# Performance work log

Measured on AMD Instinct MI355X. Metric: run time of the kernel, lower is better.

Reference implementation:

```python
import jax, jax.numpy as jnp
import numpy as np

B, S, E, H, A, D, V, L = 64, 196, 512, 512, 256, 512, 32000, 32
PAD_IDX = 2


def setup_inputs() -> dict:
    key = jax.random.key(0)
    ks = jax.random.split(key, 20)
    sc = 0.02
    return {
        "encoder_out": jax.random.normal(ks[0], (B, S, E), jnp.float32),
        "pooled": jax.random.normal(ks[1], (B, E), jnp.float32),
        "targets": jax.random.randint(ks[2], (B, L), 0, V, jnp.int64),
        "embedding": jax.random.normal(ks[3], (V, D), jnp.float32) * sc,
        "W_enc": jax.random.normal(ks[4], (A, E), jnp.float32) * sc,
        "b_enc": jnp.zeros((A,), jnp.float32),
        "W_dec": jax.random.normal(ks[5], (A, H), jnp.float32) * sc,
        "b_dec": jnp.zeros((A,), jnp.float32),
        "W_score": jax.random.normal(ks[6], (1, A), jnp.float32) * sc,
        "b_score": jnp.zeros((1,), jnp.float32),
        "W_ih": jax.random.normal(ks[7], (3 * H, D + E), jnp.float32) * sc,
        "W_hh": jax.random.normal(ks[8], (3 * H, H), jnp.float32) * sc,
        "b_ih": jnp.zeros((3 * H,), jnp.float32),
        "b_hh": jnp.zeros((3 * H,), jnp.float32),
        "W_out": jax.random.normal(ks[9], (V, H), jnp.float32) * sc,
        "b_out": jnp.zeros((V,), jnp.float32),
        "W_init": jax.random.normal(ks[10], (H, E), jnp.float32) * sc,
        "b_init": jnp.zeros((H,), jnp.float32),
    }


def reference(encoder_out, pooled, targets, embedding, W_enc, b_enc, W_dec,
              b_dec, W_score, b_score, W_ih, W_hh, b_ih, b_hh, W_out, b_out,
              W_init, b_init):
    # padding_idx=2: that embedding row is zero
    emb_tab = embedding.at[PAD_IDX].set(0.0)
    # initial hidden state from pooled features
    h0 = jnp.tanh(pooled @ W_init.T + b_init)              # (B, H)
    # encoder projection is step-invariant; hoist out of the loop
    enc_proj = jnp.einsum('bse,ae->bsa', encoder_out, W_enc) + b_enc  # (B,S,A)
    # teacher forcing (ratio=1.0): inputs are targets[:, :-1]
    tokens = targets[:, :-1].T                              # (L-1, B)

    def step(h, tok):
        embedded = emb_tab[tok]                             # (B, D)
        # Bahdanau attention
        dec_proj = h @ W_dec.T + b_dec                      # (B, A)
        energy = jnp.tanh(enc_proj + dec_proj[:, None, :])  # (B, S, A)
        scores = jnp.einsum('bsa,a->bs', energy, W_score[0]) + b_score[0]
        weights = jax.nn.softmax(scores, axis=1)            # (B, S)
        context = jnp.einsum('bs,bse->be', weights, encoder_out)  # (B, E)
        # GRU cell (PyTorch gate ordering: r, z, n)
        x = jnp.concatenate([embedded, context], axis=1)    # (B, D+E)
        gi = x @ W_ih.T + b_ih                              # (B, 3H)
        gh = h @ W_hh.T + b_hh                              # (B, 3H)
        gi_r, gi_z, gi_n = jnp.split(gi, 3, axis=1)
        gh_r, gh_z, gh_n = jnp.split(gh, 3, axis=1)
        r = jax.nn.sigmoid(gi_r + gh_r)
        z = jax.nn.sigmoid(gi_z + gh_z)
        n = jnp.tanh(gi_n + r * gh_n)
        h_new = (1.0 - z) * n + z * h
        logits = h_new @ W_out.T + b_out                    # (B, V)
        return h_new, logits

    _, logits = jax.lax.scan(step, h0, tokens)              # (L-1, B, V)
    return jnp.transpose(logits, (1, 0, 2))                 # (B, L-1, V)
```

## Files before the change

kernel.cpp:

```cpp
#include <hip/hip_runtime.h>

using bf16x8 = __attribute__((ext_vector_type(8))) short;
using f32x4  = __attribute__((ext_vector_type(4))) float;

__device__ inline float bf2f(unsigned short h){
  union { unsigned int u; float f; } v; v.u = ((unsigned int)h) << 16; return v.f;
}
__device__ inline unsigned short f2b(float x){
  union { float f; unsigned int u; } v; v.f = x;
  unsigned int r = (v.u + 0x7FFFu + ((v.u >> 16) & 1u)) >> 16;
  return (unsigned short)r;
}

__global__ void conv_k(const float* __restrict__ s, unsigned short* __restrict__ d, int n){
  int i = (blockIdx.x * 256 + threadIdx.x) * 4;
  if (i >= n) return;
  float4 v = *(const float4*)(s + i);
  unsigned int p0 = (unsigned int)f2b(v.x) | ((unsigned int)f2b(v.y) << 16);
  unsigned int p1 = (unsigned int)f2b(v.z) | ((unsigned int)f2b(v.w) << 16);
  *(uint2*)(d + i) = make_uint2(p0, p1);
}

__global__ void embed_k(const int* __restrict__ tgt, const float* __restrict__ emb,
                        unsigned short* __restrict__ out, int n){
  int idx = blockIdx.x * 256 + threadIdx.x;
  if (idx >= n) return;
  int d = idx & 511, m = idx >> 9, t = m >> 6, b = m & 63;
  int tok = tgt[b * 32 + t];
  float v = (tok == 2) ? 0.f : emb[(long)tok * 512 + d];
  out[idx] = f2b(v);
}

#define EPI_PLAIN 0
#define EPI_TANH  1
#define EPI_OUT   2

template<int EPI, bool AF32>
__global__ __launch_bounds__(256)
void gemm_bt(const void* __restrict__ Av, int lda,
             const unsigned short* __restrict__ Bp, int ldb,
             const float* __restrict__ bias,
             float* __restrict__ Cf, unsigned short* __restrict__ Cb, int ldc,
             int K,
             int n_split, const void* __restrict__ A2v,
             const unsigned short* __restrict__ B2p, int lda2, int ldb2)
{
  __shared__ __align__(16) unsigned short As[64][40];
  __shared__ __align__(16) unsigned short Bs[256][40];

  int m0 = blockIdx.x * 64;
  int n0 = blockIdx.y * 256;
  const void* Ap = Av; const unsigned short* Bq = Bp;
  int la = lda, lb = ldb, nB = n0;
  if (n_split > 0 && n0 >= n_split){ Ap = A2v; Bq = B2p; la = lda2; lb = ldb2; nB = n0 - n_split; }

  int tid  = threadIdx.x;
  int wave = tid >> 6, lane = tid & 63, quad = lane >> 4, lrow = lane & 15;

  f32x4 acc[4][4];
#pragma unroll
  for (int i = 0; i < 4; ++i)
#pragma unroll
    for (int j = 0; j < 4; ++j)
#pragma unroll
      for (int r = 0; r < 4; ++r) acc[i][j][r] = 0.f;

  int ar = tid >> 2, ac = (tid & 3) * 8;

  for (int k0 = 0; k0 < K; k0 += 32){
    if (AF32){
      const float* A32 = (const float*)Ap;
      const float4* src = (const float4*)(A32 + (long)(m0 + ar) * la + k0 + ac);
      float4 x0 = src[0], x1 = src[1];
      unsigned int p0 = (unsigned int)f2b(x0.x) | ((unsigned int)f2b(x0.y) << 16);
      unsigned int p1 = (unsigned int)f2b(x0.z) | ((unsigned int)f2b(x0.w) << 16);
      unsigned int p2 = (unsigned int)f2b(x1.x) | ((unsigned int)f2b(x1.y) << 16);
      unsigned int p3 = (unsigned int)f2b(x1.z) | ((unsigned int)f2b(x1.w) << 16);
      *(uint4*)&As[ar][ac] = make_uint4(p0, p1, p2, p3);
    } else {
      const unsigned short* A16 = (const unsigned short*)Ap;
      *(uint4*)&As[ar][ac] = *(const uint4*)(A16 + (long)(m0 + ar) * la + k0 + ac);
    }
#pragma unroll
    for (int c = 0; c < 4; ++c){
      int id = tid + c * 256; int br = id >> 2, bc = (id & 3) * 8;
      *(uint4*)&Bs[br][bc] = *(const uint4*)(Bq + (long)(nB + br) * lb + k0 + bc);
    }
    __syncthreads();

    bf16x8 af[4], bfr[4];
#pragma unroll
    for (int mf = 0; mf < 4; ++mf) af[mf]  = *(const bf16x8*)&As[mf * 16 + lrow][quad * 8];
#pragma unroll
    for (int nf = 0; nf < 4; ++nf) bfr[nf] = *(const bf16x8*)&Bs[wave * 64 + nf * 16 + lrow][quad * 8];
#pragma unroll
    for (int mf = 0; mf < 4; ++mf)
#pragma unroll
      for (int nf = 0; nf < 4; ++nf)
        acc[mf][nf] = __builtin_amdgcn_mfma_f32_16x16x32_bf16(af[mf], bfr[nf], acc[mf][nf], 0, 0, 0);
    __syncthreads();
  }

#pragma unroll
  for (int mf = 0; mf < 4; ++mf){
#pragma unroll
    for (int nf = 0; nf < 4; ++nf){
#pragma unroll
      for (int r = 0; r < 4; ++r){
        int m = m0 + mf * 16 + quad * 4 + r;
        int n = n0 + wave * 64 + nf * 16 + lrow;
        float v = acc[mf][nf][r];
        if (bias) v += bias[n];
        if (EPI == EPI_TANH){
          v = tanhf(v);
          Cf[(long)m * ldc + n] = v;
          Cb[(long)m * ldc + n] = f2b(v);
        } else if (EPI == EPI_OUT){
          Cf[(long)(m & 63) * (31 * 32000) + (long)(m >> 6) * 32000 + n] = v;
        } else {
          Cf[(long)m * ldc + n] = v;
        }
      }
    }
  }
}

__global__ __launch_bounds__(512)
void attn_step(const float* __restrict__ enc_proj,
               const float* __restrict__ enc_out,
               const float* __restrict__ W_score,
               const float* __restrict__ b_dec,
               const float* __restrict__ b_hh,
               const float* __restrict__ gi_emb,
               const float* __restrict__ giq,
               float* __restrict__ h_all,
               unsigned short* __restrict__ h_b16,
               const unsigned short* __restrict__ Wdec,
               unsigned short* __restrict__ ctx_b16,
               int t, int do_gates, int do_attn)
{
  int b = blockIdx.x, tid = threadIdx.x;
  __shared__ float sh_h[512];
  __shared__ float sdp[256];
  __shared__ float sbuf[512];
  __shared__ float sw[256];
  __shared__ float sred[512];
  __shared__ float swsc[256];

  float hv;
  if (do_gates){
    int j = tid;
    long ge = ((long)(t - 1) * 64 + b) * 1536;
    long gq = (long)b * 3072;
    float gir = gi_emb[ge + j]        + giq[gq + j];
    float giz = gi_emb[ge + 512 + j]  + giq[gq + 512 + j];
    float gin = gi_emb[ge + 1024 + j] + giq[gq + 1024 + j];
    float ghr = giq[gq + 1536 + j]        + b_hh[j];
    float ghz = giq[gq + 1536 + 512 + j]  + b_hh[512 + j];
    float ghn = giq[gq + 1536 + 1024 + j] + b_hh[1024 + j];
    float rr = 1.f / (1.f + __expf(-(gir + ghr)));
    float zz = 1.f / (1.f + __expf(-(giz + ghz)));
    float nn = tanhf(gin + rr * ghn);
    float hp = h_all[((long)(t - 1) * 64 + b) * 512 + j];
    hv = (1.f - zz) * nn + zz * hp;
    h_all[((long)t * 64 + b) * 512 + j] = hv;
    h_b16[((long)t * 64 + b) * 512 + j] = f2b(hv);
  } else {
    hv = h_all[((long)t * 64 + b) * 512 + tid];
  }
  sh_h[tid] = hv;
  if (tid < 256) swsc[tid] = W_score[tid];
  __syncthreads();
  if (!do_attn) return;

  {
    int a = tid & 255, half = tid >> 8;
    const uint4* wp = (const uint4*)(Wdec + a * 512 + half * 256);
    const float* hp = &sh_h[half * 256];
    float acc = 0.f;
#pragma unroll 8
    for (int c = 0; c < 32; ++c){
      uint4 wv = wp[c];
      acc += hp[c*8+0] * bf2f((unsigned short)(wv.x & 0xffff));
      acc += hp[c*8+1] * bf2f((unsigned short)(wv.x >> 16));
      acc += hp[c*8+2] * bf2f((unsigned short)(wv.y & 0xffff));
      acc += hp[c*8+3] * bf2f((unsigned short)(wv.y >> 16));
      acc += hp[c*8+4] * bf2f((unsigned short)(wv.z & 0xffff));
      acc += hp[c*8+5] * bf2f((unsigned short)(wv.z >> 16));
      acc += hp[c*8+6] * bf2f((unsigned short)(wv.w & 0xffff));
      acc += hp[c*8+7] * bf2f((unsigned short)(wv.w >> 16));
    }
    sbuf[tid] = acc;
    __syncthreads();
    if (tid < 256) sdp[tid] = sbuf[tid] + sbuf[tid + 256] + b_dec[tid];
    __syncthreads();
  }

  {
    int s = tid & 255, half = tid >> 8;
    float acc = 0.f;
    if (s < 196){
      const float* ep = enc_proj + ((long)b * 196 + s) * 256 + half * 128;
      const float* dp = &sdp[half * 128];
      const float* wv = &swsc[half * 128];
#pragma unroll 4
      for (int a = 0; a < 128; ++a){
        float x = ep[a] + dp[a];
        float e = __expf(2.f * x);
        acc += wv[a] * (1.f - 2.f / (e + 1.f));
      }
    }
    sbuf[tid] = acc;
    __syncthreads();
    float sc = (tid < 196) ? (sbuf[tid] + sbuf[tid + 256]) : -1e30f;
    sred[tid] = sc; __syncthreads();
    for (int off = 256; off > 0; off >>= 1){
      if (tid < off) sred[tid] = fmaxf(sred[tid], sred[tid + off]);
      __syncthreads();
    }
    float mx = sred[0]; __syncthreads();
    float e = (tid < 196) ? __expf(sc - mx) : 0.f;
    sred[tid] = e; __syncthreads();
    for (int off = 256; off > 0; off >>= 1){
      if (tid < off) sred[tid] += sred[tid + off];
      __syncthreads();
    }
    float inv = 1.f / sred[0];
    if (tid < 196) sw[tid] = e * inv;
    __syncthreads();
  }

  {
    const float* ep = enc_out + (long)b * 196 * 512 + tid;
    float acc = 0.f;
#pragma unroll 4
    for (int s = 0; s < 196; ++s) acc += sw[s] * ep[(long)s * 512];
    ctx_b16[b * 512 + tid] = f2b(acc);
  }
}

extern "C" void kernel_launch(void* const* d_in, const int* in_sizes, int n_in,
                              void* d_out, int out_size, void* d_ws, size_t ws_size,
                              hipStream_t stream)
{
  (void)in_sizes; (void)n_in; (void)out_size; (void)ws_size;
  const float* encoder_out = (const float*)d_in[0];
  const float* pooled      = (const float*)d_in[1];
  const int*   targets     = (const int*)d_in[2];
  const float* embedding   = (const float*)d_in[3];
  const float* W_enc  = (const float*)d_in[4];
  const float* b_enc  = (const float*)d_in[5];
  const float* W_dec  = (const float*)d_in[6];
  const float* b_dec  = (const float*)d_in[7];
  const float* W_score= (const float*)d_in[8];
  const float* W_ih   = (const float*)d_in[10];
  const float* W_hh   = (const float*)d_in[11];
  const float* b_ih   = (const float*)d_in[12];
  const float* b_hh   = (const float*)d_in[13];
  const float* W_out  = (const float*)d_in[14];
  const float* b_out  = (const float*)d_in[15];
  const float* W_init = (const float*)d_in[16];
  const float* b_init = (const float*)d_in[17];
  float* out = (float*)d_out;

  char* w = (char*)d_ws;
  float* enc_proj         = (float*)w;          w += 12845056;
  float* gi_emb           = (float*)w;          w += 12189696;
  float* h_all            = (float*)w;          w += 4194304;
  unsigned short* h_b16   = (unsigned short*)w; w += 2097152;
  float* giq              = (float*)w;          w += 786432;
  unsigned short* ctx_b16 = (unsigned short*)w; w += 65536;
  unsigned short* emb_b16 = (unsigned short*)w; w += 2031616;
  unsigned short* Wout_b  = (unsigned short*)w; w += 32768000;
  unsigned short* Wih_b   = (unsigned short*)w; w += 3145728;
  unsigned short* Whh_b   = (unsigned short*)w; w += 1572864;
  unsigned short* Wdec_b  = (unsigned short*)w; w += 262144;
  unsigned short* Winit_b = (unsigned short*)w; w += 524288;
  unsigned short* Wenc_b  = (unsigned short*)w; w += 262144;

  auto conv = [&](const float* s, unsigned short* d, int n){
    conv_k<<<dim3((n / 4 + 255) / 256), dim3(256), 0, stream>>>(s, d, n);
  };
  conv(W_out,  Wout_b,  32000 * 512);
  conv(W_ih,   Wih_b,   1536 * 1024);
  conv(W_hh,   Whh_b,   1536 * 512);
  conv(W_dec,  Wdec_b,  256 * 512);
  conv(W_init, Winit_b, 512 * 512);
  conv(W_enc,  Wenc_b,  256 * 512);
  embed_k<<<dim3((1984 * 512) / 256), dim3(256), 0, stream>>>(targets, embedding, emb_b16, 1984 * 512);

  gemm_bt<EPI_TANH, true><<<dim3(1, 2), 256, 0, stream>>>(
      pooled, 512, Winit_b, 512, b_init, h_all, h_b16, 512, 512, 0, nullptr, nullptr, 0, 0);
  gemm_bt<EPI_PLAIN, true><<<dim3(196, 1), 256, 0, stream>>>(
      encoder_out, 512, Wenc_b, 512, b_enc, enc_proj, nullptr, 256, 512, 0, nullptr, nullptr, 0, 0);
  gemm_bt<EPI_PLAIN, false><<<dim3(31, 6), 256, 0, stream>>>(
      emb_b16, 512, Wih_b, 1024, b_ih, gi_emb, nullptr, 1536, 512, 0, nullptr, nullptr, 0, 0);

  for (int t = 0; t < 31; ++t){
    attn_step<<<dim3(64), dim3(512), 0, stream>>>(
        enc_proj, encoder_out, W_score, b_dec, b_hh, gi_emb, giq,
        h_all, h_b16, Wdec_b, ctx_b16, t, (t > 0) ? 1 : 0, 1);
    gemm_bt<EPI_PLAIN, false><<<dim3(1, 12), 256, 0, stream>>>(
        ctx_b16, 512, Wih_b + 512, 1024, nullptr, giq, nullptr, 3072, 512,
        1536, h_b16 + (long)t * 64 * 512, Whh_b, 512, 512);
  }
  attn_step<<<dim3(64), dim3(512), 0, stream>>>(
      enc_proj, encoder_out, W_score, b_dec, b_hh, gi_emb, giq,
      h_all, h_b16, Wdec_b, ctx_b16, 31, 1, 0);

  gemm_bt<EPI_OUT, false><<<dim3(31, 125), 256, 0, stream>>>(
      h_b16 + 64 * 512, 512, Wout_b, 512, b_out, out, nullptr, 0, 512,
      0, nullptr, nullptr, 0, 0);
}
```

Before: 2.382 ms.

## Store encoder features in bf16 and stage enc_proj in swizzled LDS for attention

The encoder projection and encoder_out are now stored as bf16 instead of fp32, which halves the bytes the 31 per-step attention kernels read. Each block stages its enc_proj slice into XOR-swizzled shared memory. W_dec is transposed so the dec_proj loads coalesce across threads. Softmax reductions switch from tree reductions over shared memory to wave shuffles, and the context sum is split across two halves of the sequence. Precision drops to bf16 for these activations, and the large LDS footprint (about 100KB) limits each CU to one block.

Measured after the change: 2.167 ms. -9.0%, faster.

```diff
diff --git a/kernel.cpp b/kernel.cpp
--- a/kernel.cpp
+++ b/kernel.cpp
@@ -11,6 +11,8 @@
   unsigned int r = (v.u + 0x7FFFu + ((v.u >> 16) & 1u)) >> 16;
   return (unsigned short)r;
 }
+__device__ inline float blo(unsigned int u){ union{unsigned int v; float f;} t; t.v = u << 16; return t.f; }
+__device__ inline float bhi(unsigned int u){ union{unsigned int v; float f;} t; t.v = u & 0xffff0000u; return t.f; }
 
 __global__ void conv_k(const float* __restrict__ s, unsigned short* __restrict__ d, int n){
   int i = (blockIdx.x * 256 + threadIdx.x) * 4;
@@ -19,6 +21,12 @@
   unsigned int p0 = (unsigned int)f2b(v.x) | ((unsigned int)f2b(v.y) << 16);
   unsigned int p1 = (unsigned int)f2b(v.z) | ((unsigned int)f2b(v.w) << 16);
   *(uint2*)(d + i) = make_uint2(p0, p1);
+}
+
+__global__ void wdect_k(const float* __restrict__ Wd, unsigned short* __restrict__ o){
+  int idx = blockIdx.x * 256 + threadIdx.x;
+  int k = idx >> 8, a = idx & 255;
+  o[idx] = f2b(Wd[a * 512 + k]);
 }
 
 __global__ void embed_k(const int* __restrict__ tgt, const float* __restrict__ emb,
@@ -34,6 +42,7 @@
 #define EPI_PLAIN 0
 #define EPI_TANH  1
 #define EPI_OUT   2
+#define EPI_B16   3
 
 template<int EPI, bool AF32>
 __global__ __launch_bounds__(256)
@@ -117,6 +126,8 @@
           Cb[(long)m * ldc + n] = f2b(v);
         } else if (EPI == EPI_OUT){
           Cf[(long)(m & 63) * (31 * 32000) + (long)(m >> 6) * 32000 + n] = v;
+        } else if (EPI == EPI_B16){
+          Cb[(long)m * ldc + n] = f2b(v);
         } else {
           Cf[(long)m * ldc + n] = v;
         }
@@ -126,8 +137,8 @@
 }
 
 __global__ __launch_bounds__(512)
-void attn_step(const float* __restrict__ enc_proj,
-               const float* __restrict__ enc_out,
+void attn_step(const uint4* __restrict__ ep4,
+               const unsigned int* __restrict__ eo2,
                const float* __restrict__ W_score,
                const float* __restrict__ b_dec,
                const float* __restrict__ b_hh,
@@ -135,17 +146,19 @@
                const float* __restrict__ giq,
                float* __restrict__ h_all,
                unsigned short* __restrict__ h_b16,
-               const unsigned short* __restrict__ Wdec,
+               const uint2* __restrict__ WdecT4,
                unsigned short* __restrict__ ctx_b16,
                int t, int do_gates, int do_attn)
 {
+  __shared__ __align__(16) uint4 ep_s4[6272];
+  __shared__ float sh_h[512];
+  __shared__ float2 dpw[256];
+  __shared__ float spart[2048];
+  __shared__ float sw[256];
+  __shared__ float wred[16];
+
   int b = blockIdx.x, tid = threadIdx.x;
-  __shared__ float sh_h[512];
-  __shared__ float sdp[256];
-  __shared__ float sbuf[512];
-  __shared__ float sw[256];
-  __shared__ float sred[512];
-  __shared__ float swsc[256];
+  int lane = tid & 63, wv = tid >> 6;
 
   float hv;
   if (do_gates){
@@ -168,74 +181,101 @@
   } else {
     hv = h_all[((long)t * 64 + b) * 512 + tid];
   }
+  if (!do_attn) return;
+
   sh_h[tid] = hv;
-  if (tid < 256) swsc[tid] = W_score[tid];
-  __syncthreads();
-  if (!do_attn) return;
-
-  {
-    int a = tid & 255, half = tid >> 8;
-    const uint4* wp = (const uint4*)(Wdec + a * 512 + half * 256);
-    const float* hp = &sh_h[half * 256];
-    float acc = 0.f;
-#pragma unroll 8
-    for (int c = 0; c < 32; ++c){
-      uint4 wv = wp[c];
-      acc += hp[c*8+0] * bf2f((unsigned short)(wv.x & 0xffff));
-      acc += hp[c*8+1] * bf2f((unsigned short)(wv.x >> 16));
-      acc += hp[c*8+2] * bf2f((unsigned short)(wv.y & 0xffff));
-      acc += hp[c*8+3] * bf2f((unsigned short)(wv.y >> 16));
-      acc += hp[c*8+4] * bf2f((unsigned short)(wv.z & 0xffff));
-      acc += hp[c*8+5] * bf2f((unsigned short)(wv.z >> 16));
-      acc += hp[c*8+6] * bf2f((unsigned short)(wv.w & 0xffff));
-      acc += hp[c*8+7] * bf2f((unsigned short)(wv.w >> 16));
-    }
-    sbuf[tid] = acc;
-    __syncthreads();
-    if (tid < 256) sdp[tid] = sbuf[tid] + sbuf[tid + 256] + b_dec[tid];
-    __syncthreads();
-  }
+  float wsc = (tid < 256) ? W_score[tid] : 0.f;
+
+  {
+    const uint4* src = ep4 + (long)b * 6272;
+    for (int c = tid; c < 6272; c += 512){
+      int r = c >> 5, col = c & 31;
+      ep_s4[(r << 5) | (col ^ (r & 7))] = src[c];
+    }
+  }
+  __syncthreads();
+
+  {
+    int a4 = tid & 63, kg = tid >> 6;
+    const uint2* wp = WdecT4 + ((kg << 12) | a4);
+    const float* hp = &sh_h[kg << 6];
+    float ac0 = 0.f, ac1 = 0.f, ac2 = 0.f, ac3 = 0.f;
+#pragma unroll 16
+    for (int kk = 0; kk < 64; ++kk){
+      uint2 wq = wp[kk << 6];
+      float hk = hp[kk];
+      ac0 += hk * blo(wq.x); ac1 += hk * bhi(wq.x);
+      ac2 += hk * blo(wq.y); ac3 += hk * bhi(wq.y);
+    }
+    *(float4*)&spart[(kg << 8) | (a4 << 2)] = make_float4(ac0, ac1, ac2, ac3);
+  }
+  __syncthreads();
+  if (tid < 256){
+    float dp = b_dec[tid];
+#pragma unroll
+    for (int kg = 0; kg < 8; ++kg) dp += spart[(kg << 8) | tid];
+    dpw[tid] = make_float2(dp, wsc);
+  }
+  __syncthreads();
 
   {
     int s = tid & 255, half = tid >> 8;
     float acc = 0.f;
     if (s < 196){
-      const float* ep = enc_proj + ((long)b * 196 + s) * 256 + half * 128;
-      const float* dp = &sdp[half * 128];
-      const float* wv = &swsc[half * 128];
+      int rb = s << 5, sx = s & 7;
 #pragma unroll 4
-      for (int a = 0; a < 128; ++a){
-        float x = ep[a] + dp[a];
-        float e = __expf(2.f * x);
-        acc += wv[a] * (1.f - 2.f / (e + 1.f));
+      for (int j = 0; j < 16; ++j){
+        uint4 v = ep_s4[rb | (((half << 4) | j) ^ sx)];
+        int aj = (half << 7) | (j << 3);
+#define SCP(uu, ab) { \
+        float2 dA = dpw[ab], dB = dpw[(ab) + 1]; \
+        float xA = blo(uu) + dA.x, xB = bhi(uu) + dB.x; \
+        float eA = __expf(2.f * xA), eB = __expf(2.f * xB); \
+        acc += dA.y * (1.f - 2.f / (eA + 1.f)); \
+        acc += dB.y * (1.f - 2.f / (eB + 1.f)); }
+        SCP(v.x, aj) SCP(v.y, aj + 2) SCP(v.z, aj + 4) SCP(v.w, aj + 6)
+#undef SCP
       }
     }
-    sbuf[tid] = acc;
-    __syncthreads();
-    float sc = (tid < 196) ? (sbuf[tid] + sbuf[tid + 256]) : -1e30f;
-    sred[tid] = sc; __syncthreads();
-    for (int off = 256; off > 0; off >>= 1){
-      if (tid < off) sred[tid] = fmaxf(sred[tid], sred[tid + off]);
-      __syncthreads();
-    }
-    float mx = sred[0]; __syncthreads();
-    float e = (tid < 196) ? __expf(sc - mx) : 0.f;
-    sred[tid] = e; __syncthreads();
-    for (int off = 256; off > 0; off >>= 1){
-      if (tid < off) sred[tid] += sred[tid + off];
-      __syncthreads();
-    }
-    float inv = 1.f / sred[0];
-    if (tid < 196) sw[tid] = e * inv;
-    __syncthreads();
-  }
-
-  {
-    const float* ep = enc_out + (long)b * 196 * 512 + tid;
-    float acc = 0.f;
-#pragma unroll 4
-    for (int s = 0; s < 196; ++s) acc += sw[s] * ep[(long)s * 512];
-    ctx_b16[b * 512 + tid] = f2b(acc);
+    spart[tid] = acc;
+  }
+  __syncthreads();
+
+  float sc = -1e30f, ee = 0.f;
+  if (tid < 256) sc = (tid < 196) ? (spart[tid] + spart[tid + 256]) : -1e30f;
+  float mm = sc;
+#pragma unroll
+  for (int off = 32; off >= 1; off >>= 1) mm = fmaxf(mm, __shfl_xor(mm, off));
+  if (tid < 256 && lane == 0) wred[wv] = mm;
+  __syncthreads();
+  float mx = fmaxf(fmaxf(wred[0], wred[1]), fmaxf(wred[2], wred[3]));
+  if (tid < 256){
+    ee = (tid < 196) ? __expf(sc - mx) : 0.f;
+    sw[tid] = ee;
+  }
+  float ss = ee;
+#pragma unroll
+  for (int off = 32; off >= 1; off >>= 1) ss += __shfl_xor(ss, off);
+  if (tid < 256 && lane == 0) wred[8 + wv] = ss;
+  __syncthreads();
+  float inv = 1.f / (wred[8] + wred[9] + wred[10] + wred[11]);
+
+  {
+    int e2 = tid & 255, sh2 = tid >> 8;
+    const unsigned int* src = eo2 + ((long)b * 196 + sh2 * 98) * 256 + e2;
+    float a0 = 0.f, a1 = 0.f;
+#pragma unroll 2
+    for (int s2 = 0; s2 < 98; ++s2){
+      unsigned int v = src[(long)s2 * 256];
+      float w = sw[sh2 * 98 + s2];
+      a0 += w * blo(v); a1 += w * bhi(v);
+    }
+    *(float2*)&spart[(sh2 << 9) | (e2 << 1)] = make_float2(a0, a1);
+  }
+  __syncthreads();
+  {
+    float cv = (spart[tid] + spart[tid + 512]) * inv;
+    ctx_b16[(b << 9) | tid] = f2b(cv);
   }
 }
 
@@ -264,7 +304,7 @@
   float* out = (float*)d_out;
 
   char* w = (char*)d_ws;
-  float* enc_proj         = (float*)w;          w += 12845056;
+  unsigned short* eo_b16  = (unsigned short*)w; w += 12845056;
   float* gi_emb           = (float*)w;          w += 12189696;
   float* h_all            = (float*)w;          w += 4194304;
   unsigned short* h_b16   = (unsigned short*)w; w += 2097152;
@@ -274,9 +314,10 @@
   unsigned short* Wout_b  = (unsigned short*)w; w += 32768000;
   unsigned short* Wih_b   = (unsigned short*)w; w += 3145728;
   unsigned short* Whh_b   = (unsigned short*)w; w += 1572864;
-  unsigned short* Wdec_b  = (unsigned short*)w; w += 262144;
+  unsigned short* WdecT_b = (unsigned short*)w; w += 262144;
   unsigned short* Winit_b = (unsigned short*)w; w += 524288;
   unsigned short* Wenc_b  = (unsigned short*)w; w += 262144;
+  unsigned short* ep_b16  = (unsigned short*)w; w += 6422528;
 
   auto conv = [&](const float* s, unsigned short* d, int n){
     conv_k<<<dim3((n / 4 + 255) / 256), dim3(256), 0, stream>>>(s, d, n);
@@ -284,29 +325,31 @@
   conv(W_out,  Wout_b,  32000 * 512);
   conv(W_ih,   Wih_b,   1536 * 1024);
   conv(W_hh,   Whh_b,   1536 * 512);
-  conv(W_dec,  Wdec_b,  256 * 512);
   conv(W_init, Winit_b, 512 * 512);
   conv(W_enc,  Wenc_b,  256 * 512);
+  conv(encoder_out, eo_b16, 64 * 196 * 512);
+  wdect_k<<<dim3(512), dim3(256), 0, stream>>>(W_dec, WdecT_b);
   embed_k<<<dim3((1984 * 512) / 256), dim3(256), 0, stream>>>(targets, embedding, emb_b16, 1984 * 512);
 
   gemm_bt<EPI_TANH, true><<<dim3(1, 2), 256, 0, stream>>>(
       pooled, 512, Winit_b, 512, b_init, h_all, h_b16, 512, 512, 0, nullptr, nullptr, 0, 0);
-  gemm_bt<EPI_PLAIN, true><<<dim3(196, 1), 256, 0, stream>>>(
-      encoder_out, 512, Wenc_b, 512, b_enc, enc_proj, nullptr, 256, 512, 0, nullptr, nullptr, 0, 0);
+  gemm_bt<EPI_B16, true><<<dim3(196, 1), 256, 0, stream>>>(
+      encoder_out, 512, Wenc_b, 512, b_enc, nullptr, ep_b16, 256, 512, 0, nullptr, nullptr, 0, 0);
   gemm_bt<EPI_PLAIN, false><<<dim3(31, 6), 256, 0, stream>>>(
       emb_b16, 512, Wih_b, 1024, b_ih, gi_emb, nullptr, 1536, 512, 0, nullptr, nullptr, 0, 0);
 
   for (int t = 0; t < 31; ++t){
     attn_step<<<dim3(64), dim3(512), 0, stream>>>(
-        enc_proj, encoder_out, W_score, b_dec, b_hh, gi_emb, giq,
-        h_all, h_b16, Wdec_b, ctx_b16, t, (t > 0) ? 1 : 0, 1);
+        (const uint4*)ep_b16, (const unsigned int*)eo_b16, W_score, b_dec, b_hh,
+        gi_emb, giq, h_all, h_b16, (const uint2*)WdecT_b, ctx_b16,
+        t, (t > 0) ? 1 : 0, 1);
     gemm_bt<EPI_PLAIN, false><<<dim3(1, 12), 256, 0, stream>>>(
         ctx_b16, 512, Wih_b + 512, 1024, nullptr, giq, nullptr, 3072, 512,
         1536, h_b16 + (long)t * 64 * 512, Whh_b, 512, 512);
   }
   attn_step<<<dim3(64), dim3(512), 0, stream>>>(
-      enc_proj, encoder_out, W_score, b_dec, b_hh, gi_emb, giq,
-      h_all, h_b16, Wdec_b, ctx_b16, 31, 1, 0);
+      (const uint4*)ep_b16, (const unsigned int*)eo_b16, W_score, b_dec, b_hh,
+      gi_emb, giq, h_all, h_b16, (const uint2*)WdecT_b, ctx_b16, 31, 1, 0);
 
   gemm_bt<EPI_OUT, false><<<dim3(31, 125), 256, 0, stream>>>(
       h_b16 + 64 * 512, 512, Wout_b, 512, b_out, out, nullptr, 0, 512,
```
